# Kernel tuning notes

Hardware: AMD Instinct MI355X
Metric: run time of the kernel (lower is better)

The kernel has to match this reference:

```python
import jax, jax.numpy as jnp
import numpy as np

N = 100000
E = 1000000
EMB = 128
HID = 128
LABELS = 2048


def gcn_conv(x, W, b, row, col, ew, num_nodes):
    """PyG GCNConv: add self-loops (weight 1), symmetric gcn_norm, x@W, scatter-add, +bias."""
    loop = jnp.arange(num_nodes, dtype=row.dtype)
    row2 = jnp.concatenate([row, loop])
    col2 = jnp.concatenate([col, loop])
    ew2 = jnp.concatenate([ew, jnp.ones((num_nodes,), dtype=ew.dtype)])
    deg = jax.ops.segment_sum(ew2, col2, num_segments=num_nodes)  # [N]
    dinv = jnp.where(deg > 0, jax.lax.rsqrt(deg), 0.0)
    norm = dinv[row2] * ew2 * dinv[col2]                          # [E+N]
    h = x @ W                                                     # [N, out]
    msg = h[row2] * norm[:, None]                                 # [E+N, out]
    out = jax.ops.segment_sum(msg, col2, num_segments=num_nodes)  # [N, out]
    return out + b


def setup_inputs() -> dict:
    key = jax.random.key(0)
    ks = jax.random.split(key, 9)
    return {
        "node_indices": jnp.arange(N, dtype=jnp.int64 if jax.config.jax_enable_x64 else jnp.int32),
        "edge_index": jax.random.randint(ks[0], (2, E), 0, N),
        "edge_weight": jax.random.uniform(ks[1], (E,), dtype=jnp.float32),
        "emb": jax.random.normal(ks[2], (N, EMB), dtype=jnp.float32),
        "W1": jax.random.normal(ks[3], (EMB, HID), dtype=jnp.float32) * (1.0 / np.sqrt(EMB)),
        "b1": jnp.zeros((HID,), dtype=jnp.float32),
        "W2": jax.random.normal(ks[4], (HID, HID), dtype=jnp.float32) * (1.0 / np.sqrt(HID)),
        "b2": jnp.zeros((HID,), dtype=jnp.float32),
        "Wout": jax.random.normal(ks[5], (HID, LABELS), dtype=jnp.float32) * (1.0 / np.sqrt(HID)),
        "bout": jnp.zeros((LABELS,), dtype=jnp.float32),
    }


def reference(node_indices, edge_index, edge_weight, emb, W1, b1, W2, b2, Wout, bout):
    row, col = edge_index[0], edge_index[1]
    x = emb[node_indices]                                   # embedding lookup [N, EMB]
    x = jax.nn.relu(gcn_conv(x, W1, b1, row, col, edge_weight, N))
    # dropout p=0.5 is identity in eval mode
    x = jax.nn.relu(gcn_conv(x, W2, b2, row, col, edge_weight, N))
    return x @ Wout + bout                                  # [N, LABELS]
```

## Files before the change

### kernel.cpp

```cpp
#include <hip/hip_runtime.h>
#include <hip/hip_bf16.h>
#include <stdint.h>

#define NN 100000
#define NE 1000000
#define DIM 128
#define NLAB 2048

typedef __attribute__((ext_vector_type(8))) short bf16x8;
typedef __attribute__((ext_vector_type(4))) float f32x4;
typedef __attribute__((ext_vector_type(2))) unsigned short us2;
typedef __attribute__((ext_vector_type(4))) unsigned short us4;
typedef __attribute__((ext_vector_type(8))) unsigned short us8;

__device__ __forceinline__ unsigned short f2bf(float f){
    union { float f; unsigned int u; } v; v.f = f;
    unsigned int r = v.u + 0x7FFFu + ((v.u >> 16) & 1u);
    return (unsigned short)(r >> 16);
}
__device__ __forceinline__ float bf2f(unsigned short b){
    union { unsigned int u; float f; } v; v.u = ((unsigned int)b) << 16;
    return v.f;
}

__global__ void k_init(int* __restrict__ cnt, float* __restrict__ deg){
    int i = blockIdx.x*256 + threadIdx.x;
    if(i < NN){ cnt[i] = 0; deg[i] = 1.0f; }
}

__global__ void k_count(const int* __restrict__ col, const float* __restrict__ ew,
                        int* __restrict__ cnt, float* __restrict__ deg){
    int e = blockIdx.x*256 + threadIdx.x;
    if(e < NE){
        int c = col[e];
        atomicAdd(&cnt[c], 1);
        atomicAdd(&deg[c], ew[e]);
    }
}

__global__ void k_scan1(const int* __restrict__ cnt, int* __restrict__ excl,
                        int* __restrict__ bsum){
    __shared__ int s[256];
    int tid = threadIdx.x;
    int i = blockIdx.x*256 + tid;
    int v = (i < NN) ? cnt[i] : 0;
    int x = v;
    s[tid] = x; __syncthreads();
    for(int off=1; off<256; off<<=1){
        int t = (tid >= off) ? s[tid-off] : 0;
        __syncthreads();
        x += t; s[tid] = x;
        __syncthreads();
    }
    if(i < NN) excl[i] = x - v;
    if(tid == 255) bsum[blockIdx.x] = x;
}

__global__ void k_scan2(const int* __restrict__ bsum, int* __restrict__ bsumx, int nb){
    __shared__ int s[512];
    int tid = threadIdx.x;
    int v = (tid < nb) ? bsum[tid] : 0;
    int x = v;
    s[tid] = x; __syncthreads();
    for(int off=1; off<512; off<<=1){
        int t = (tid >= off) ? s[tid-off] : 0;
        __syncthreads();
        x += t; s[tid] = x;
        __syncthreads();
    }
    if(tid < nb) bsumx[tid] = x - v;
}

__global__ void k_scan3(const int* __restrict__ excl, const int* __restrict__ bsumx,
                        int* __restrict__ start, int* __restrict__ cursor){
    int i = blockIdx.x*256 + threadIdx.x;
    if(i < NN){
        int v = excl[i] + bsumx[blockIdx.x];
        start[i] = v; cursor[i] = v;
    }
    if(i == 0) start[NN] = NE;
}

__global__ void k_dinv(const float* __restrict__ deg, float* __restrict__ dinv){
    int i = blockIdx.x*256 + threadIdx.x;
    if(i < NN){ float d = deg[i]; dinv[i] = d > 0.f ? rsqrtf(d) : 0.f; }
}

__global__ void k_fill(const int* __restrict__ row, const int* __restrict__ col,
                       const float* __restrict__ ew, int* __restrict__ cursor,
                       int* __restrict__ csrc, float* __restrict__ cw){
    int e = blockIdx.x*256 + threadIdx.x;
    if(e < NE){
        int c = col[e];
        int p = atomicAdd(&cursor[c], 1);
        csrc[p] = row[e];
        cw[p]   = ew[e];
    }
}

__global__ void k_gather(const int* __restrict__ ni, const float* __restrict__ emb,
                         unsigned short* __restrict__ xbf){
    int id = blockIdx.x*256 + threadIdx.x;
    if(id >= NN*32) return;
    int i = id >> 5, q = (id & 31) << 2;
    float4 v = *reinterpret_cast<const float4*>(&emb[(long)ni[i]*DIM + q]);
    us4 o; o.x = f2bf(v.x); o.y = f2bf(v.y); o.z = f2bf(v.z); o.w = f2bf(v.w);
    *reinterpret_cast<us4*>(&xbf[(long)i*DIM + q]) = o;
}

__global__ __launch_bounds__(256) void k_gemm128(const unsigned short* __restrict__ X,
                                                 const float* __restrict__ W,
                                                 unsigned short* __restrict__ H){
    __shared__ unsigned short Wt[DIM][DIM+8];
    int tid = threadIdx.x;
    #pragma unroll
    for(int t=0; t<64; ++t){
        int idx = tid + t*256;
        int k = idx >> 7, j = idx & 127;
        Wt[j][k] = f2bf(W[k*DIM + j]);
    }
    __syncthreads();

    int lane = tid & 63, w = tid >> 6;
    int rowbase = blockIdx.x*64 + w*16;
    int r16 = lane & 15, ksel = lane >> 4;
    int arow = rowbase + r16; if(arow > NN-1) arow = NN-1;
    const unsigned short* xr = X + (long)arow*DIM;
    bf16x8 a[4];
    #pragma unroll
    for(int ks=0; ks<4; ++ks)
        a[ks] = *reinterpret_cast<const bf16x8*>(&xr[ks*32 + ksel*8]);

    f32x4 acc[8] = {};
    #pragma unroll
    for(int ks=0; ks<4; ++ks){
        #pragma unroll
        for(int nt=0; nt<8; ++nt){
            bf16x8 b = *reinterpret_cast<const bf16x8*>(&Wt[nt*16 + r16][ks*32 + ksel*8]);
            acc[nt] = __builtin_amdgcn_mfma_f32_16x16x32_bf16(a[ks], b, acc[nt], 0, 0, 0);
        }
    }

    int orow0 = rowbase + ksel*4;
    #pragma unroll
    for(int nt=0; nt<8; ++nt){
        int oc = nt*16 + r16;
        #pragma unroll
        for(int r=0; r<4; ++r){
            int orow = orow0 + r;
            if(orow < NN) H[(long)orow*DIM + oc] = f2bf(acc[nt][r]);
        }
    }
}

__global__ void k_agg(const unsigned short* __restrict__ H, const int* __restrict__ start,
                      const int* __restrict__ csrc, const float* __restrict__ cw,
                      const float* __restrict__ dinv, const float* __restrict__ bias,
                      unsigned short* __restrict__ Xo){
    int wid  = (blockIdx.x*256 + threadIdx.x) >> 6;
    int lane = threadIdx.x & 63;
    if(wid >= NN) return;
    int c = wid;
    int q = lane >> 4;
    int f = lane & 15;
    int s = start[c], e = start[c+1];
    float acc[8] = {0.f,0.f,0.f,0.f,0.f,0.f,0.f,0.f};
    for(int p=s; p<e; p+=4){
        int pe = p + q;
        bool valid = pe < e;
        int pc = valid ? pe : e-1;
        int r = csrc[pc];
        float sc = cw[pc] * dinv[r];
        if(!valid) sc = 0.f;
        us8 hv = *reinterpret_cast<const us8*>(&H[(long)r*DIM + f*8]);
        #pragma unroll
        for(int j=0;j<8;++j) acc[j] += sc * bf2f(hv[j]);
    }
    #pragma unroll
    for(int j=0;j<8;++j){
        acc[j] += __shfl_xor(acc[j], 16);
        acc[j] += __shfl_xor(acc[j], 32);
    }
    if(q == 0){
        float dc = dinv[c];
        us8 hc = *reinterpret_cast<const us8*>(&H[(long)c*DIM + f*8]);
        us8 o;
        #pragma unroll
        for(int j=0;j<8;++j){
            float v = dc*(acc[j] + dc*bf2f(hc[j])) + bias[f*8+j];
            v = v > 0.f ? v : 0.f;
            o[j] = f2bf(v);
        }
        *reinterpret_cast<us8*>(&Xo[(long)c*DIM + f*8]) = o;
    }
}

__global__ __launch_bounds__(256) void k_wt(const float* __restrict__ W,
                                            unsigned short* __restrict__ Wt){
    __shared__ float t[32][33];
    int kb = blockIdx.x & 3;
    int cb = blockIdx.x >> 2;
    int ci = threadIdx.x & 31;
    int k0 = threadIdx.x >> 5;
    #pragma unroll
    for(int p=0; p<4; ++p){
        int ki = k0 + p*8;
        t[ki][ci] = W[(long)(kb*32+ki)*NLAB + cb*32 + ci];
    }
    __syncthreads();
    int kk = threadIdx.x & 31;
    int c0 = threadIdx.x >> 5;
    #pragma unroll
    for(int p=0; p<4; ++p){
        int cc = c0 + p*8;
        Wt[(long)(cb*32+cc)*DIM + kb*32 + kk] = f2bf(t[kk][cc]);
    }
}

#define RT_PER_BLK 4
__global__ __launch_bounds__(256) void k_gemm_out(const unsigned short* __restrict__ X,
                                                  const unsigned short* __restrict__ Wt,
                                                  const float* __restrict__ bout,
                                                  float* __restrict__ out){
    __shared__ unsigned short Wl[128*136];
    int bid = blockIdx.x;
    int colg = bid & 15;
    int rtg  = bid >> 4;
    int colbase = colg * 128;
    int tid = threadIdx.x;

    #pragma unroll
    for(int i=0; i<8; ++i){
        int chunk = i*256 + tid;
        int r = chunk >> 4, seg = chunk & 15;
        bf16x8 v = *reinterpret_cast<const bf16x8*>(Wt + (long)(colbase + r)*DIM + seg*8);
        *reinterpret_cast<bf16x8*>(&Wl[r*136 + seg*8]) = v;
    }
    __syncthreads();

    int lane = tid & 63, w = tid >> 6;
    int r16 = lane & 15, ksel = lane >> 4;

    #pragma unroll 1
    for(int it=0; it<RT_PER_BLK; ++it){
        int rowbase = (rtg*RT_PER_BLK + it)*64 + w*16;
        int row = rowbase + r16;
        int arow = row < NN ? row : NN-1;

        const unsigned short* xr = X + (long)arow*DIM + ksel*8;
        bf16x8 b[4];
        #pragma unroll
        for(int ks=0; ks<4; ++ks)
            b[ks] = *reinterpret_cast<const bf16x8*>(xr + ks*32);

        f32x4 acc[8] = {};
        #pragma unroll
        for(int nt=0; nt<8; ++nt){
            const unsigned short* wl = &Wl[(nt*16 + r16)*136 + ksel*8];
            #pragma unroll
            for(int ks=0; ks<4; ++ks){
                bf16x8 a = *reinterpret_cast<const bf16x8*>(wl + ks*32);
                acc[nt] = __builtin_amdgcn_mfma_f32_16x16x32_bf16(a, b[ks], acc[nt], 0, 0, 0);
            }
        }

        if(row < NN){
            float* orow = out + (long)row*NLAB + colbase + ksel*4;
            const float* br = bout + colbase + ksel*4;
            #pragma unroll
            for(int nt=0; nt<8; ++nt){
                f32x4 bv = *reinterpret_cast<const f32x4*>(br + nt*16);
                f32x4 v = acc[nt] + bv;
                __builtin_nontemporal_store(v, reinterpret_cast<f32x4*>(orow + nt*16));
            }
        }
    }
}

extern "C" void kernel_launch(void* const* d_in, const int* in_sizes, int n_in,
                              void* d_out, int out_size, void* d_ws, size_t ws_size,
                              hipStream_t stream){
    const int*   ni  = (const int*)  d_in[0];
    const int*   ei  = (const int*)  d_in[1];
    const float* ew  = (const float*)d_in[2];
    const float* emb = (const float*)d_in[3];
    const float* W1  = (const float*)d_in[4];
    const float* b1  = (const float*)d_in[5];
    const float* W2  = (const float*)d_in[6];
    const float* b2  = (const float*)d_in[7];
    const float* Wo  = (const float*)d_in[8];
    const float* bo  = (const float*)d_in[9];
    float* out = (float*)d_out;
    const int* row = ei;
    const int* col = ei + NE;

    char* ws = (char*)d_ws;
    size_t off = 0;
    auto alloc = [&](size_t bytes){ void* p = ws + off; off += (bytes + 255) & ~size_t(255); return p; };
    int*   cnt    = (int*)  alloc((size_t)NN*4);
    int*   excl   = (int*)  alloc((size_t)NN*4);
    int*   bsum   = (int*)  alloc(512*4);
    int*   bsumx  = (int*)  alloc(512*4);
    int*   start  = (int*)  alloc((size_t)(NN+1)*4);
    int*   cursor = (int*)  alloc((size_t)NN*4);
    float* deg    = (float*)alloc((size_t)NN*4);
    float* dinv   = (float*)alloc((size_t)NN*4);
    int*   csrc   = (int*)  alloc((size_t)NE*4);
    float* cw     = (float*)alloc((size_t)NE*4);
    unsigned short* Xbf = (unsigned short*)alloc((size_t)NN*DIM*2);
    unsigned short* Hbf = (unsigned short*)alloc((size_t)NN*DIM*2);
    unsigned short* Wot = (unsigned short*)alloc((size_t)NLAB*DIM*2);

    const int nbN = (NN + 255)/256;
    const int nbE = (NE + 255)/256;

    k_init <<<nbN, 256, 0, stream>>>(cnt, deg);
    k_count<<<nbE, 256, 0, stream>>>(col, ew, cnt, deg);
    k_scan1<<<nbN, 256, 0, stream>>>(cnt, excl, bsum);
    k_scan2<<<1,   512, 0, stream>>>(bsum, bsumx, nbN);
    k_scan3<<<nbN, 256, 0, stream>>>(excl, bsumx, start, cursor);
    k_dinv <<<nbN, 256, 0, stream>>>(deg, dinv);
    k_fill <<<nbE, 256, 0, stream>>>(row, col, ew, cursor, csrc, cw);

    k_gather<<<(NN*32 + 255)/256, 256, 0, stream>>>(ni, emb, Xbf);
    k_wt    <<<256, 256, 0, stream>>>(Wo, Wot);

    k_gemm128<<<(NN+63)/64, 256, 0, stream>>>(Xbf, W1, Hbf);
    k_agg    <<<(NN*64+255)/256, 256, 0, stream>>>(Hbf, start, csrc, cw, dinv, b1, Xbf);
    k_gemm128<<<(NN+63)/64, 256, 0, stream>>>(Xbf, W2, Hbf);
    k_agg    <<<(NN*64+255)/256, 256, 0, stream>>>(Hbf, start, csrc, cw, dinv, b2, Xbf);
    {
        int rowtiles = (NN + 63)/64;
        int rtg = (rowtiles + RT_PER_BLK - 1)/RT_PER_BLK;
        k_gemm_out<<<rtg*16, 256, 0, stream>>>(Xbf, Wot, bo, out);
    }
}
```

Baseline: 514.5 us.

## Merge setup kernels, unroll aggregation loop, prefetch rows and remap blocks in output GEMM

```diff
diff --git a/kernel.cpp b/kernel.cpp
--- a/kernel.cpp
+++ b/kernel.cpp
@@ -23,9 +23,47 @@
     return v.f;
 }
 
-__global__ void k_init(int* __restrict__ cnt, float* __restrict__ deg){
-    int i = blockIdx.x*256 + threadIdx.x;
-    if(i < NN){ cnt[i] = 0; deg[i] = 1.0f; }
+#define NB_GATHER 12500
+#define NB_WT 256
+#define NB_INIT 391
+__global__ __launch_bounds__(256) void k_setup(const int* __restrict__ ni,
+                                               const float* __restrict__ emb,
+                                               unsigned short* __restrict__ xbf,
+                                               const float* __restrict__ W,
+                                               unsigned short* __restrict__ Wt,
+                                               int* __restrict__ cnt,
+                                               float* __restrict__ deg){
+    __shared__ float t[32][33];
+    int b = blockIdx.x;
+    if(b < NB_GATHER){
+        int id = b*256 + threadIdx.x;
+        int i = id >> 5, q = (id & 31) << 2;
+        float4 v = *reinterpret_cast<const float4*>(&emb[(long)ni[i]*DIM + q]);
+        us4 o; o.x = f2bf(v.x); o.y = f2bf(v.y); o.z = f2bf(v.z); o.w = f2bf(v.w);
+        *reinterpret_cast<us4*>(&xbf[(long)i*DIM + q]) = o;
+    } else if(b < NB_GATHER + NB_WT){
+        int bb = b - NB_GATHER;
+        int kb = bb & 3;
+        int cb = bb >> 2;
+        int ci = threadIdx.x & 31;
+        int k0 = threadIdx.x >> 5;
+        #pragma unroll
+        for(int p=0; p<4; ++p){
+            int ki = k0 + p*8;
+            t[ki][ci] = W[(long)(kb*32+ki)*NLAB + cb*32 + ci];
+        }
+        __syncthreads();
+        int kk = threadIdx.x & 31;
+        int c0 = threadIdx.x >> 5;
+        #pragma unroll
+        for(int p=0; p<4; ++p){
+            int cc = c0 + p*8;
+            Wt[(long)(cb*32+cc)*DIM + kb*32 + kk] = f2bf(t[kk][cc]);
+        }
+    } else {
+        int i = (b - NB_GATHER - NB_WT)*256 + threadIdx.x;
+        if(i < NN){ cnt[i] = 0; deg[i] = 1.0f; }
+    }
 }
 
 __global__ void k_count(const int* __restrict__ col, const float* __restrict__ ew,
@@ -72,18 +110,16 @@
 }
 
 __global__ void k_scan3(const int* __restrict__ excl, const int* __restrict__ bsumx,
-                        int* __restrict__ start, int* __restrict__ cursor){
+                        int* __restrict__ start, int* __restrict__ cursor,
+                        const float* __restrict__ deg, float* __restrict__ dinv){
     int i = blockIdx.x*256 + threadIdx.x;
     if(i < NN){
         int v = excl[i] + bsumx[blockIdx.x];
         start[i] = v; cursor[i] = v;
+        float d = deg[i];
+        dinv[i] = d > 0.f ? rsqrtf(d) : 0.f;
     }
     if(i == 0) start[NN] = NE;
-}
-
-__global__ void k_dinv(const float* __restrict__ deg, float* __restrict__ dinv){
-    int i = blockIdx.x*256 + threadIdx.x;
-    if(i < NN){ float d = deg[i]; dinv[i] = d > 0.f ? rsqrtf(d) : 0.f; }
 }
 
 __global__ void k_fill(const int* __restrict__ row, const int* __restrict__ col,
@@ -96,16 +132,6 @@
         csrc[p] = row[e];
         cw[p]   = ew[e];
     }
-}
-
-__global__ void k_gather(const int* __restrict__ ni, const float* __restrict__ emb,
-                         unsigned short* __restrict__ xbf){
-    int id = blockIdx.x*256 + threadIdx.x;
-    if(id >= NN*32) return;
-    int i = id >> 5, q = (id & 31) << 2;
-    float4 v = *reinterpret_cast<const float4*>(&emb[(long)ni[i]*DIM + q]);
-    us4 o; o.x = f2bf(v.x); o.y = f2bf(v.y); o.z = f2bf(v.z); o.w = f2bf(v.w);
-    *reinterpret_cast<us4*>(&xbf[(long)i*DIM + q]) = o;
 }
 
 __global__ __launch_bounds__(256) void k_gemm128(const unsigned short* __restrict__ X,
@@ -165,16 +191,20 @@
     int f = lane & 15;
     int s = start[c], e = start[c+1];
     float acc[8] = {0.f,0.f,0.f,0.f,0.f,0.f,0.f,0.f};
-    for(int p=s; p<e; p+=4){
-        int pe = p + q;
-        bool valid = pe < e;
-        int pc = valid ? pe : e-1;
-        int r = csrc[pc];
-        float sc = cw[pc] * dinv[r];
-        if(!valid) sc = 0.f;
-        us8 hv = *reinterpret_cast<const us8*>(&H[(long)r*DIM + f*8]);
-        #pragma unroll
-        for(int j=0;j<8;++j) acc[j] += sc * bf2f(hv[j]);
+    for(int p=s; p<e; p+=8){
+        int pe0 = p + q, pe1 = p + q + 4;
+        int pc0 = pe0 < e ? pe0 : e-1;
+        int pc1 = pe1 < e ? pe1 : e-1;
+        int r0 = csrc[pc0];
+        int r1 = csrc[pc1];
+        float sc0 = cw[pc0] * dinv[r0];
+        float sc1 = cw[pc1] * dinv[r1];
+        if(pe0 >= e) sc0 = 0.f;
+        if(pe1 >= e) sc1 = 0.f;
+        us8 h0 = *reinterpret_cast<const us8*>(&H[(long)r0*DIM + f*8]);
+        us8 h1 = *reinterpret_cast<const us8*>(&H[(long)r1*DIM + f*8]);
+        #pragma unroll
+        for(int j=0;j<8;++j) acc[j] += sc0 * bf2f(h0[j]) + sc1 * bf2f(h1[j]);
     }
     #pragma unroll
     for(int j=0;j<8;++j){
@@ -195,37 +225,16 @@
     }
 }
 
-__global__ __launch_bounds__(256) void k_wt(const float* __restrict__ W,
-                                            unsigned short* __restrict__ Wt){
-    __shared__ float t[32][33];
-    int kb = blockIdx.x & 3;
-    int cb = blockIdx.x >> 2;
-    int ci = threadIdx.x & 31;
-    int k0 = threadIdx.x >> 5;
-    #pragma unroll
-    for(int p=0; p<4; ++p){
-        int ki = k0 + p*8;
-        t[ki][ci] = W[(long)(kb*32+ki)*NLAB + cb*32 + ci];
-    }
-    __syncthreads();
-    int kk = threadIdx.x & 31;
-    int c0 = threadIdx.x >> 5;
-    #pragma unroll
-    for(int p=0; p<4; ++p){
-        int cc = c0 + p*8;
-        Wt[(long)(cb*32+cc)*DIM + kb*32 + kk] = f2bf(t[kk][cc]);
-    }
-}
-
 #define RT_PER_BLK 4
+#define GRID_OUT 6256
 __global__ __launch_bounds__(256) void k_gemm_out(const unsigned short* __restrict__ X,
                                                   const unsigned short* __restrict__ Wt,
                                                   const float* __restrict__ bout,
                                                   float* __restrict__ out){
     __shared__ unsigned short Wl[128*136];
-    int bid = blockIdx.x;
-    int colg = bid & 15;
-    int rtg  = bid >> 4;
+    int obid = (blockIdx.x & 7)*(GRID_OUT/8) + (blockIdx.x >> 3);
+    int colg = obid & 15;
+    int rtg  = obid >> 4;
     int colbase = colg * 128;
     int tid = threadIdx.x;
 
@@ -241,17 +250,29 @@
     int lane = tid & 63, w = tid >> 6;
     int r16 = lane & 15, ksel = lane >> 4;
 
+    int row0 = (rtg*RT_PER_BLK + 0)*64 + w*16 + r16;
+    {
+        int arow = row0 < NN ? row0 : NN-1;
+        (void)arow;
+    }
+    bf16x8 bcur[4], bnext[4];
+    {
+        int arow = row0 < NN ? row0 : NN-1;
+        const unsigned short* xr = X + (long)arow*DIM + ksel*8;
+        #pragma unroll
+        for(int ks=0; ks<4; ++ks) bcur[ks] = *reinterpret_cast<const bf16x8*>(xr + ks*32);
+    }
+
     #pragma unroll 1
     for(int it=0; it<RT_PER_BLK; ++it){
-        int rowbase = (rtg*RT_PER_BLK + it)*64 + w*16;
-        int row = rowbase + r16;
-        int arow = row < NN ? row : NN-1;
-
-        const unsigned short* xr = X + (long)arow*DIM + ksel*8;
-        bf16x8 b[4];
-        #pragma unroll
-        for(int ks=0; ks<4; ++ks)
-            b[ks] = *reinterpret_cast<const bf16x8*>(xr + ks*32);
+        int row = (rtg*RT_PER_BLK + it)*64 + w*16 + r16;
+        if(it+1 < RT_PER_BLK){
+            int rown = row + 64;
+            int arow = rown < NN ? rown : NN-1;
+            const unsigned short* xr = X + (long)arow*DIM + ksel*8;
+            #pragma unroll
+            for(int ks=0; ks<4; ++ks) bnext[ks] = *reinterpret_cast<const bf16x8*>(xr + ks*32);
+        }
 
         f32x4 acc[8] = {};
         #pragma unroll
@@ -260,7 +281,7 @@
             #pragma unroll
             for(int ks=0; ks<4; ++ks){
                 bf16x8 a = *reinterpret_cast<const bf16x8*>(wl + ks*32);
-                acc[nt] = __builtin_amdgcn_mfma_f32_16x16x32_bf16(a, b[ks], acc[nt], 0, 0, 0);
+                acc[nt] = __builtin_amdgcn_mfma_f32_16x16x32_bf16(a, bcur[ks], acc[nt], 0, 0, 0);
             }
         }
 
@@ -274,6 +295,8 @@
                 __builtin_nontemporal_store(v, reinterpret_cast<f32x4*>(orow + nt*16));
             }
         }
+        #pragma unroll
+        for(int ks=0; ks<4; ++ks) bcur[ks] = bnext[ks];
     }
 }
 
@@ -314,24 +337,16 @@
     const int nbN = (NN + 255)/256;
     const int nbE = (NE + 255)/256;
 
-    k_init <<<nbN, 256, 0, stream>>>(cnt, deg);
+    k_setup<<<NB_GATHER + NB_WT + NB_INIT, 256, 0, stream>>>(ni, emb, Xbf, Wo, Wot, cnt, deg);
     k_count<<<nbE, 256, 0, stream>>>(col, ew, cnt, deg);
     k_scan1<<<nbN, 256, 0, stream>>>(cnt, excl, bsum);
     k_scan2<<<1,   512, 0, stream>>>(bsum, bsumx, nbN);
-    k_scan3<<<nbN, 256, 0, stream>>>(excl, bsumx, start, cursor);
-    k_dinv <<<nbN, 256, 0, stream>>>(deg, dinv);
+    k_scan3<<<nbN, 256, 0, stream>>>(excl, bsumx, start, cursor, deg, dinv);
     k_fill <<<nbE, 256, 0, stream>>>(row, col, ew, cursor, csrc, cw);
-
-    k_gather<<<(NN*32 + 255)/256, 256, 0, stream>>>(ni, emb, Xbf);
-    k_wt    <<<256, 256, 0, stream>>>(Wo, Wot);
 
     k_gemm128<<<(NN+63)/64, 256, 0, stream>>>(Xbf, W1, Hbf);
     k_agg    <<<(NN*64+255)/256, 256, 0, stream>>>(Hbf, start, csrc, cw, dinv, b1, Xbf);
     k_gemm128<<<(NN+63)/64, 256, 0, stream>>>(Xbf, W2, Hbf);
     k_agg    <<<(NN*64+255)/256, 256, 0, stream>>>(Hbf, start, csrc, cw, dinv, b2, Xbf);
-    {
-        int rowtiles = (NN + 63)/64;
-        int rtg = (rowtiles + RT_PER_BLK - 1)/RT_PER_BLK;
-        k_gemm_out<<<rtg*16, 256, 0, stream>>>(Xbf, Wot, bo, out);
-    }
-}
+    k_gemm_out<<<GRID_OUT, 256, 0, stream>>>(Xbf, Wot, bo, out);
+}
```

Result: faster. 489.9 us (-4.8%).
